# Kernel optimization log

Hardware: AMD Instinct MI355X
Metric: run time of the kernel (lower is better)

## Reference

```python
import jax, jax.numpy as jnp
import numpy as np

N_NODES = 50000
N_EDGES = 625000
D = 128          # hidden_dim
H = 8            # num_heads
DH = D // H      # head_dim
L = 4            # num_layers
F_IN = 64        # in_channels
G = 64           # num graphs
BETA = 1.0
EPS = 1e-5       # layernorm eps


def _seg_softmax(s, idx, n):
    # softmax of s over segments defined by idx (segments present in idx are never empty)
    m = jax.ops.segment_max(s, idx, num_segments=n)
    e = jnp.exp(s - m[idx])
    d = jax.ops.segment_sum(e, idx, num_segments=n)
    return e / d[idx]


def _ln(x, s, b):
    mu = jnp.mean(x, axis=-1, keepdims=True)
    var = jnp.var(x, axis=-1, keepdims=True)
    return (x - mu) / jnp.sqrt(var + EPS) * s + b


def _forward(x, edge_index, batch, node_W, node_b, cW1, cb1, cW2, cb2,
             qW, qb, kW, kb, vW, vb, oW, ob, bW, bb,
             f1W, f1b, f2W, f2b, n1s, n1b, n2s, n2b,
             outW1, outb1, outW2, outb2):
    N = x.shape[0]
    src, tgt = edge_index[0], edge_index[1]
    h = x @ node_W + node_b                              # [N, D]
    for l in range(L):
        # ---- dynamic curvature (attention-approximated Wasserstein) ----
        h_src, h_tgt = h[src], h[tgt]                    # [E, D]
        sim = jnp.sum(h_src * h_tgt, axis=-1) * BETA     # [E]
        alpha = _seg_softmax(sim, tgt, N)                # segment softmax over tgt
        dist = jnp.linalg.norm(h_src - h_tgt, axis=-1)   # [E]
        agg = jax.ops.segment_sum(alpha * dist, tgt, num_segments=N)
        curv = 1.0 - agg[tgt] / jnp.maximum(dist, 1e-6)  # [E]
        ce = jax.nn.relu(curv[:, None] @ cW1 + cb1) @ cW2 + cb2  # [E, D]
        # ---- CurvphormerLayer ----
        xn = _ln(h, n1s[l], n1b[l])
        q = (xn @ qW[l] + qb[l]).reshape(N, H, DH)
        k = (xn @ kW[l] + kb[l]).reshape(N, H, DH)
        v = (xn @ vW[l] + vb[l]).reshape(N, H, DH)
        scores = jnp.sum(q[src] * k[tgt], axis=-1) / (DH ** 0.5)  # [E, H]
        scores = scores + ce @ bW[l] + bb[l]                       # curvature bias
        probs = _seg_softmax(scores, tgt, N)                       # [E, H]
        msgs = (probs[..., None] * v[tgt]).reshape(-1, D)          # [E, D]
        aggm = jax.ops.segment_sum(msgs, src, num_segments=N)     # scatter to src
        h = h + (aggm @ oW[l] + ob[l])
        xn2 = _ln(h, n2s[l], n2b[l])
        h = h + (jax.nn.relu(xn2 @ f1W[l] + f1b[l]) @ f2W[l] + f2b[l])
    # ---- mean pool per graph ----
    counts = jnp.maximum(jax.ops.segment_sum(jnp.ones((N,), h.dtype), batch, num_segments=G), 1.0)
    g = jax.ops.segment_sum(h, batch, num_segments=G) / counts[:, None]
    return jax.nn.relu(g @ outW1 + outb1) @ outW2 + outb2


def setup_inputs() -> dict:
    keys = iter(jax.random.split(jax.random.key(0), 32))
    p = lambda shape, s=0.02: jax.random.normal(next(keys), shape, jnp.float32) * s
    x = jax.random.normal(next(keys), (N_NODES, F_IN), jnp.float32)
    edge_index = jax.random.randint(next(keys), (2, N_EDGES), 0, N_NODES)
    batch = jnp.sort(jax.random.randint(next(keys), (N_NODES,), 0, G))
    inp = {
        "x": x, "edge_index": edge_index, "batch": batch,
        "node_W": p((F_IN, D)), "node_b": p((D,)),
        "cW1": p((1, D)), "cb1": p((D,)), "cW2": p((D, D)), "cb2": p((D,)),
        "qW": p((L, D, D)), "qb": p((L, D)),
        "kW": p((L, D, D)), "kb": p((L, D)),
        "vW": p((L, D, D)), "vb": p((L, D)),
        "oW": p((L, D, D)), "ob": p((L, D)),
        "bW": p((L, D, H)), "bb": p((L, H)),
        "f1W": p((L, D, 4 * D)), "f1b": p((L, 4 * D)),
        "f2W": p((L, 4 * D, D)), "f2b": p((L, D)),
        "n1s": jnp.ones((L, D), jnp.float32), "n1b": jnp.zeros((L, D), jnp.float32),
        "n2s": jnp.ones((L, D), jnp.float32), "n2b": jnp.zeros((L, D), jnp.float32),
        "outW1": p((D, D // 2)), "outb1": p((D // 2,)),
        "outW2": p((D // 2, 1)), "outb2": p((1,)),
    }
    return inp


def reference(x, edge_index, batch, node_W, node_b, cW1, cb1, cW2, cb2,
              qW, qb, kW, kb, vW, vb, oW, ob, bW, bb,
              f1W, f1b, f2W, f2b, n1s, n1b, n2s, n2b,
              outW1, outb1, outW2, outb2):
    return _forward(x, edge_index, batch, node_W, node_b, cW1, cb1, cW2, cb2,
                    qW, qb, kW, kb, vW, vb, oW, ob, bW, bb,
                    f1W, f1b, f2W, f2b, n1s, n1b, n2s, n2b,
                    outW1, outb1, outW2, outb2)
```

## Files before the change

kernel.cpp:

```cpp
#include <hip/hip_runtime.h>

#define NN 50000
#define NE 625000
#define DD 128
#define HH 8
#define DHH 16
#define NL 4
#define FIN 64
#define NG 64
#define LN_EPS 1e-5f
#define NSEG 129
#define NT32 1563
#define NT64 782
#define NT4 12500
#define NBS 196
#define HLP 132

typedef __bf16 bf16x8_t __attribute__((ext_vector_type(8)));
typedef unsigned short ushort8_t __attribute__((ext_vector_type(8)));
typedef float f32x4_t __attribute__((ext_vector_type(4)));
union BF8 { ushort8_t u; bf16x8_t b; };

__device__ __forceinline__ void fma4(float4& a, float s, float4 w) {
  a.x = fmaf(s, w.x, a.x); a.y = fmaf(s, w.y, a.y);
  a.z = fmaf(s, w.z, a.z); a.w = fmaf(s, w.w, a.w);
}
__device__ __forceinline__ unsigned short f2bf(float f) {
  unsigned u = __float_as_uint(f);
  unsigned r = ((u >> 16) & 1u) + 0x7FFFu;
  return (unsigned short)((u + r) >> 16);
}
__device__ __forceinline__ float bf2f(unsigned short u) {
  return __uint_as_float((unsigned)u << 16);
}

__device__ __forceinline__ void ln_tile_bf32(const float* __restrict__ h, int nb,
                                             const float* __restrict__ sc,
                                             const float* __restrict__ bi,
                                             ushort* xbf) {
  int tid = threadIdx.x;
  int r = tid >> 4, l16 = tid & 15;
  int nr = nb + r; if (nr >= NN) nr = NN - 1;
  const float* hp = h + (size_t)nr * DD + l16 * 8;
  float4 a0 = *(const float4*)hp;
  float4 a1 = *(const float4*)(hp + 4);
  float sum = a0.x + a0.y + a0.z + a0.w + a1.x + a1.y + a1.z + a1.w;
  float sq  = a0.x*a0.x + a0.y*a0.y + a0.z*a0.z + a0.w*a0.w
            + a1.x*a1.x + a1.y*a1.y + a1.z*a1.z + a1.w*a1.w;
#pragma unroll
  for (int off = 8; off >= 1; off >>= 1) {
    sum += __shfl_xor(sum, off, 64);
    sq  += __shfl_xor(sq,  off, 64);
  }
  float mu   = sum * (1.0f / DD);
  float var  = sq * (1.0f / DD) - mu * mu;
  float rstd = rsqrtf(var + LN_EPS);
  int d0 = l16 * 8;
  float4 s0 = *(const float4*)(sc + d0), s1 = *(const float4*)(sc + d0 + 4);
  float4 b0 = *(const float4*)(bi + d0), b1 = *(const float4*)(bi + d0 + 4);
  ushort8_t u;
  u[0] = f2bf((a0.x - mu) * rstd * s0.x + b0.x);
  u[1] = f2bf((a0.y - mu) * rstd * s0.y + b0.y);
  u[2] = f2bf((a0.z - mu) * rstd * s0.z + b0.z);
  u[3] = f2bf((a0.w - mu) * rstd * s0.w + b0.w);
  u[4] = f2bf((a1.x - mu) * rstd * s1.x + b1.x);
  u[5] = f2bf((a1.y - mu) * rstd * s1.y + b1.y);
  u[6] = f2bf((a1.z - mu) * rstd * s1.z + b1.z);
  u[7] = f2bf((a1.w - mu) * rstd * s1.w + b1.w);
  int off = (r * 256 + l16 * 16) ^ ((r & 7) << 4);
  *(ushort8_t*)((char*)xbf + off) = u;
}

__global__ __launch_bounds__(256) void k_node_proj(const float* __restrict__ x,
                                                   const float* __restrict__ W,
                                                   const float* __restrict__ b,
                                                   float* __restrict__ h) {
  __shared__ float Wl[FIN * DD];
  __shared__ float xt[32][FIN];
  int tid = threadIdx.x;
  int nb = blockIdx.x * 32;
  for (int i = tid * 4; i < FIN * DD; i += 1024)
    *(float4*)&Wl[i] = *(const float4*)(W + i);
  for (int i = tid * 4; i < 32 * FIN; i += 1024) {
    int row = i >> 6, cc = i & 63;
    int node = nb + row; if (node >= NN) node = NN - 1;
    *(float4*)&xt[row][cc] = *(const float4*)(x + (size_t)node * FIN + cc);
  }
  __syncthreads();
  int c4 = (tid & 31) * 4;
  int r0 = (tid >> 5) * 4;
  float4 bv = *(const float4*)(b + c4);
  float4 a0 = bv, a1 = bv, a2 = bv, a3 = bv;
  for (int k = 0; k < FIN; k++) {
    float4 wv = *(const float4*)&Wl[k * DD + c4];
    fma4(a0, xt[r0][k], wv);
    fma4(a1, xt[r0 + 1][k], wv);
    fma4(a2, xt[r0 + 2][k], wv);
    fma4(a3, xt[r0 + 3][k], wv);
  }
  int n0 = nb + r0;
  if (n0 < NN)     *(float4*)(h + (size_t)n0 * DD + c4) = a0;
  if (n0 + 1 < NN) *(float4*)(h + (size_t)(n0 + 1) * DD + c4) = a1;
  if (n0 + 2 < NN) *(float4*)(h + (size_t)(n0 + 2) * DD + c4) = a2;
  if (n0 + 3 < NN) *(float4*)(h + (size_t)(n0 + 3) * DD + c4) = a3;
}

__global__ __launch_bounds__(256) void k_edge1(const int* __restrict__ src_s, const int* __restrict__ tgt_s,
                                               const float* __restrict__ h, float* __restrict__ sim,
                                               float* __restrict__ dist) {
  int gid = blockIdx.x * 256 + threadIdx.x;
  int e = gid >> 4;
  if (e >= NE) return;
  int j = gid & 15;
  int s = src_s[e], t = tgt_s[e];
  const float4* ap = (const float4*)(h + (size_t)s * DD + j * 8);
  const float4* bp = (const float4*)(h + (size_t)t * DD + j * 8);
  float4 a0 = ap[0], a1 = ap[1];
  float4 b0 = bp[0], b1 = bp[1];
  float dot = 0.f, sq = 0.f;
  dot = fmaf(a0.x, b0.x, dot); dot = fmaf(a0.y, b0.y, dot);
  dot = fmaf(a0.z, b0.z, dot); dot = fmaf(a0.w, b0.w, dot);
  dot = fmaf(a1.x, b1.x, dot); dot = fmaf(a1.y, b1.y, dot);
  dot = fmaf(a1.z, b1.z, dot); dot = fmaf(a1.w, b1.w, dot);
  float d0 = a0.x - b0.x, d1 = a0.y - b0.y, d2 = a0.z - b0.z, d3 = a0.w - b0.w;
  float d4 = a1.x - b1.x, d5 = a1.y - b1.y, d6 = a1.z - b1.z, d7 = a1.w - b1.w;
  sq = fmaf(d0, d0, sq); sq = fmaf(d1, d1, sq); sq = fmaf(d2, d2, sq); sq = fmaf(d3, d3, sq);
  sq = fmaf(d4, d4, sq); sq = fmaf(d5, d5, sq); sq = fmaf(d6, d6, sq); sq = fmaf(d7, d7, sq);
#pragma unroll
  for (int off = 8; off >= 1; off >>= 1) {
    dot += __shfl_xor(dot, off, 64);
    sq  += __shfl_xor(sq,  off, 64);
  }
  if (j == 0) {
    sim[e]  = dot;
    dist[e] = sqrtf(sq);
  }
}

__global__ __launch_bounds__(256) void k_curva(const int* __restrict__ rowstart_t,
    const int* __restrict__ eid_t, const float* __restrict__ sim,
    const float* __restrict__ dist, float* __restrict__ aggv) {
  int node = blockIdx.x * 32 + (threadIdx.x >> 3);
  if (node >= NN) return;
  int j = threadIdx.x & 7;
  int rs = rowstart_t[node], re = rowstart_t[node + 1];
  float m = -3.4e38f;
  for (int i = rs + j; i < re; i += 8) m = fmaxf(m, sim[eid_t[i]]);
#pragma unroll
  for (int off = 1; off <= 4; off <<= 1) m = fmaxf(m, __shfl_xor(m, off, 64));
  float den = 0.f, nd = 0.f;
  for (int i = rs + j; i < re; i += 8) {
    int e = eid_t[i];
    float ev = expf(sim[e] - m);
    den += ev;
    nd = fmaf(ev, dist[e], nd);
  }
#pragma unroll
  for (int off = 1; off <= 4; off <<= 1) {
    den += __shfl_xor(den, off, 64);
    nd  += __shfl_xor(nd,  off, 64);
  }
  if (j == 0) aggv[node] = den > 0.f ? nd / den : 0.f;
}

__global__ __launch_bounds__(512) void k_ln_qkv(const float* __restrict__ h,
    const float* __restrict__ n1s_l, const float* __restrict__ n1b_l,
    const ushort* __restrict__ qkvT_l,
    const float* __restrict__ qb_l, const float* __restrict__ kb_l, const float* __restrict__ vb_l,
    ushort* __restrict__ q, ushort* __restrict__ kk, ushort* __restrict__ v) {
  __shared__ __align__(16) ushort xbf[32 * DD];
  int nb = blockIdx.x * 32;
  ln_tile_bf32(h, nb, n1s_l, n1b_l, xbf);
  __syncthreads();
  int lane = threadIdx.x & 63;
  int w = threadIdx.x >> 6;
  int g = lane >> 4, c = lane & 15;
  int xr = (c & 7) << 4;
  char* xb = (char*)xbf;
  BF8 a[2][4];
#pragma unroll
  for (int nt = 0; nt < 2; nt++)
#pragma unroll
    for (int kt = 0; kt < 4; kt++)
      a[nt][kt].u = *(ushort8_t*)(xb + (((nt * 16 + c) * 256 + kt * 64 + g * 16) ^ xr));
#pragma unroll
  for (int ti = 0; ti < 3; ti++) {
    int t = w * 3 + ti;
    int m = t >> 3;
    int colb = (t & 7) * 16;
    const float* bias = (m == 0 ? qb_l : (m == 1 ? kb_l : vb_l));
    float4 bv = *(const float4*)(bias + colb + g * 4);
    f32x4_t acc0 = {bv.x, bv.y, bv.z, bv.w};
    f32x4_t acc1 = acc0;
    const ushort* wp = qkvT_l + (size_t)(m * DD + colb + c) * DD + g * 8;
#pragma unroll
    for (int kt = 0; kt < 4; kt++) {
      BF8 b; b.u = *(const ushort8_t*)(wp + kt * 32);
      acc0 = __builtin_amdgcn_mfma_f32_16x16x32_bf16(b.b, a[0][kt].b, acc0, 0, 0, 0);
      acc1 = __builtin_amdgcn_mfma_f32_16x16x32_bf16(b.b, a[1][kt].b, acc1, 0, 0, 0);
    }
    ushort* out = (m == 0 ? q : (m == 1 ? kk : v));
    int n0 = nb + c;
    if (n0 < NN) {
      ushort4 o; o.x = f2bf(acc0[0]); o.y = f2bf(acc0[1]); o.z = f2bf(acc0[2]); o.w = f2bf(acc0[3]);
      *(ushort4*)(out + (size_t)n0 * DD + colb + g * 4) = o;
    }
    int n1 = nb + 16 + c;
    if (n1 < NN) {
      ushort4 o; o.x = f2bf(acc1[0]); o.y = f2bf(acc1[1]); o.z = f2bf(acc1[2]); o.w = f2bf(acc1[3]);
      *(ushort4*)(out + (size_t)n1 * DD + colb + g * 4) = o;
    }
  }
}

__global__ __launch_bounds__(256) void k_scores_sm(const int* __restrict__ src_s,
    const int* __restrict__ rowstart_t, const int* __restrict__ eid_t,
    const ushort* __restrict__ q, const ushort* __restrict__ k,
    const float* __restrict__ dist, const float* __restrict__ aggv,
    const float* __restrict__ bp_g,
    const float* __restrict__ slope_l, const float* __restrict__ inter_l,
    float* __restrict__ escore, float2* __restrict__ msd) {
  __shared__ float lsl[NSEG * HH], lin[NSEG * HH], bp[DD];
  int tid = threadIdx.x;
  for (int idx = tid; idx < NSEG * HH; idx += 256) { lsl[idx] = slope_l[idx]; lin[idx] = inter_l[idx]; }
  if (tid < DD) bp[tid] = bp_g[tid];
  __syncthreads();
  int node = blockIdx.x * 4 + (tid >> 6);
  if (node >= NN) return;
  int lane = tid & 63;
  int hh = lane & 7;
  int eidx = lane >> 3;
  int rs = rowstart_t[node], re = rowstart_t[node + 1];
  float av = aggv[node];
  const ushort8_t* kp = (const ushort8_t*)(k + (size_t)node * DD + hh * DHH);
  ushort8_t k0 = kp[0], k1 = kp[1];
  float m = -3.4e38f, ssum = 0.f;
  for (int i = rs + eidx; i < re; i += 8) {
    int e = eid_t[i];
    int s = src_s[e];
    float dd = dist[e];
    const ushort8_t* qp = (const ushort8_t*)(q + (size_t)s * DD + hh * DHH);
    ushort8_t q0 = qp[0], q1 = qp[1];
    float curv = 1.0f - av / fmaxf(dd, 1e-6f);
    int lo = 0, hi = DD;
    while (lo < hi) { int mid = (lo + hi) >> 1; if (bp[mid] < curv) lo = mid + 1; else hi = mid; }
    float bias = fmaf(lsl[lo * HH + hh], curv, lin[lo * HH + hh]);
    float dot = 0.f;
#pragma unroll
    for (int jj = 0; jj < 8; jj++) dot = fmaf(bf2f(q0[jj]), bf2f(k0[jj]), dot);
#pragma unroll
    for (int jj = 0; jj < 8; jj++) dot = fmaf(bf2f(q1[jj]), bf2f(k1[jj]), dot);
    float sc = dot * 0.25f + bias;
    escore[e * HH + hh] = sc;
    float mn = fmaxf(m, sc);
    ssum = ssum * expf(m - mn) + expf(sc - mn);
    m = mn;
  }
#pragma unroll
  for (int off = 8; off <= 32; off <<= 1) {
    float m2 = __shfl_xor(m, off, 64);
    float s2 = __shfl_xor(ssum, off, 64);
    float M = fmaxf(m, m2);
    ssum = ssum * expf(m - M) + s2 * expf(m2 - M);
    m = M;
  }
  if (eidx == 0) {
    float2 o; o.x = m; o.y = ssum > 0.f ? 1.0f / ssum : 0.f;
    msd[(size_t)node * HH + hh] = o;
  }
}

__global__ __launch_bounds__(256) void k_agg(const int* __restrict__ tgt_s,
    const int* __restrict__ rowstart,
    const float* __restrict__ escore, const float2* __restrict__ msd,
    const ushort* __restrict__ v, ushort* __restrict__ aggmb) {
  int wave = (blockIdx.x * 256 + threadIdx.x) >> 6;
  int lane = threadIdx.x & 63;
  int rs = rowstart[wave], re = rowstart[wave + 1];
  int hh = lane >> 3;
  int d = lane * 2;
  float a0 = 0.f, a1 = 0.f;
  int i = rs;
  for (; i + 4 <= re; i += 4) {
    int t0 = tgt_s[i], t1 = tgt_s[i + 1], t2 = tgt_s[i + 2], t3 = tgt_s[i + 3];
    float e0 = escore[(i    ) * HH + hh];
    float e1 = escore[(i + 1) * HH + hh];
    float e2 = escore[(i + 2) * HH + hh];
    float e3 = escore[(i + 3) * HH + hh];
    float2 m0 = msd[(size_t)t0 * HH + hh], m1 = msd[(size_t)t1 * HH + hh];
    float2 m2 = msd[(size_t)t2 * HH + hh], m3 = msd[(size_t)t3 * HH + hh];
    ushort2 v0 = *(const ushort2*)(v + (size_t)t0 * DD + d);
    ushort2 v1 = *(const ushort2*)(v + (size_t)t1 * DD + d);
    ushort2 v2 = *(const ushort2*)(v + (size_t)t2 * DD + d);
    ushort2 v3 = *(const ushort2*)(v + (size_t)t3 * DD + d);
    float p0 = expf(e0 - m0.x) * m0.y;
    float p1 = expf(e1 - m1.x) * m1.y;
    float p2 = expf(e2 - m2.x) * m2.y;
    float p3 = expf(e3 - m3.x) * m3.y;
    a0 = fmaf(p0, bf2f(v0.x), a0); a1 = fmaf(p0, bf2f(v0.y), a1);
    a0 = fmaf(p1, bf2f(v1.x), a0); a1 = fmaf(p1, bf2f(v1.y), a1);
    a0 = fmaf(p2, bf2f(v2.x), a0); a1 = fmaf(p2, bf2f(v2.y), a1);
    a0 = fmaf(p3, bf2f(v3.x), a0); a1 = fmaf(p3, bf2f(v3.y), a1);
  }
  for (; i < re; i++) {
    int t = tgt_s[i];
    float2 md = msd[(size_t)t * HH + hh];
    float prob = expf(escore[i * HH + hh] - md.x) * md.y;
    ushort2 vv = *(const ushort2*)(v + (size_t)t * DD + d);
    a0 = fmaf(prob, bf2f(vv.x), a0);
    a1 = fmaf(prob, bf2f(vv.y), a1);
  }
  ushort2 o; o.x = f2bf(a0); o.y = f2bf(a1);
  *(ushort2*)(aggmb + (size_t)wave * DD + d) = o;
}

__global__ __launch_bounds__(512) void k_attn_ffn(const ushort* __restrict__ aggmb,
    const ushort* __restrict__ oT_l, const float* __restrict__ ob_l,
    const float* __restrict__ n2s_l, const float* __restrict__ n2b_l,
    const ushort* __restrict__ f1T_l, const float* __restrict__ f1b_l,
    const ushort* __restrict__ f2T_l, const float* __restrict__ f2b_l,
    float* __restrict__ h) {
  __shared__ float hL[64 * HLP];
  __shared__ __align__(16) char ubuf[64 * 128 * 2];
  char* xb = ubuf;
  char* tb = ubuf;
  int nb = blockIdx.x * 64;
  int tid = threadIdx.x;
  int lane = tid & 63, w = tid >> 6;
  int g = lane >> 4, c = lane & 15;
  int colb = w * 16;
  int xr = (c & 7) << 4;
  {
    float4 obv = *(const float4*)(ob_l + colb + g * 4);
    const ushort* wp = oT_l + (size_t)(colb + c) * DD + g * 8;
    BF8 b0, b1, b2, b3;
    b0.u = *(const ushort8_t*)(wp);
    b1.u = *(const ushort8_t*)(wp + 32);
    b2.u = *(const ushort8_t*)(wp + 64);
    b3.u = *(const ushort8_t*)(wp + 96);
#pragma unroll
    for (int nt = 0; nt < 4; nt++) {
      int node = nb + nt * 16 + c;
      int na = node < NN ? node : NN - 1;
      const ushort* ap = aggmb + (size_t)na * DD + g * 8;
      BF8 a0, a1, a2, a3;
      a0.u = *(const ushort8_t*)(ap);
      a1.u = *(const ushort8_t*)(ap + 32);
      a2.u = *(const ushort8_t*)(ap + 64);
      a3.u = *(const ushort8_t*)(ap + 96);
      f32x4_t acc = {obv.x, obv.y, obv.z, obv.w};
      acc = __builtin_amdgcn_mfma_f32_16x16x32_bf16(b0.b, a0.b, acc, 0, 0, 0);
      acc = __builtin_amdgcn_mfma_f32_16x16x32_bf16(b1.b, a1.b, acc, 0, 0, 0);
      acc = __builtin_amdgcn_mfma_f32_16x16x32_bf16(b2.b, a2.b, acc, 0, 0, 0);
      acc = __builtin_amdgcn_mfma_f32_16x16x32_bf16(b3.b, a3.b, acc, 0, 0, 0);
      float4 hv = *(const float4*)(h + (size_t)na * DD + colb + g * 4);
      hv.x += acc[0]; hv.y += acc[1]; hv.z += acc[2]; hv.w += acc[3];
      *(float4*)&hL[(nt * 16 + c) * HLP + colb + g * 4] = hv;
    }
  }
  __syncthreads();
  {
    int l16 = tid & 15;
    int d0 = l16 * 8;
    float4 s0 = *(const float4*)(n2s_l + d0), s1 = *(const float4*)(n2s_l + d0 + 4);
    float4 bb0 = *(const float4*)(n2b_l + d0), bb1 = *(const float4*)(n2b_l + d0 + 4);
#pragma unroll
    for (int p = 0; p < 2; p++) {
      int r = p * 32 + (tid >> 4);
      const float* hp = &hL[r * HLP + d0];
      float4 a0 = *(const float4*)hp;
      float4 a1 = *(const float4*)(hp + 4);
      float sum = a0.x + a0.y + a0.z + a0.w + a1.x + a1.y + a1.z + a1.w;
      float sq  = a0.x*a0.x + a0.y*a0.y + a0.z*a0.z + a0.w*a0.w
                + a1.x*a1.x + a1.y*a1.y + a1.z*a1.z + a1.w*a1.w;
#pragma unroll
      for (int off = 8; off >= 1; off >>= 1) {
        sum += __shfl_xor(sum, off, 64);
        sq  += __shfl_xor(sq,  off, 64);
      }
      float mu   = sum * (1.0f / DD);
      float var  = sq * (1.0f / DD) - mu * mu;
      float rstd = rsqrtf(var + LN_EPS);
      ushort8_t u;
      u[0] = f2bf((a0.x - mu) * rstd * s0.x + bb0.x);
      u[1] = f2bf((a0.y - mu) * rstd * s0.y + bb0.y);
      u[2] = f2bf((a0.z - mu) * rstd * s0.z + bb0.z);
      u[3] = f2bf((a0.w - mu) * rstd * s0.w + bb0.w);
      u[4] = f2bf((a1.x - mu) * rstd * s1.x + bb1.x);
      u[5] = f2bf((a1.y - mu) * rstd * s1.y + bb1.y);
      u[6] = f2bf((a1.z - mu) * rstd * s1.z + bb1.z);
      u[7] = f2bf((a1.w - mu) * rstd * s1.w + bb1.w);
      int off = (r * 256 + l16 * 16) ^ ((r & 7) << 4);
      *(ushort8_t*)(xb + off) = u;
    }
  }
  __syncthreads();
  BF8 a[4][4];
#pragma unroll
  for (int nt = 0; nt < 4; nt++)
#pragma unroll
    for (int kt = 0; kt < 4; kt++)
      a[nt][kt].u = *(ushort8_t*)(xb + (((nt * 16 + c) * 256 + kt * 64 + g * 16) ^ xr));
  __syncthreads();
  float4 bv2 = *(const float4*)(f2b_l + colb + g * 4);
  f32x4_t o0 = {bv2.x, bv2.y, bv2.z, bv2.w};
  f32x4_t o1 = o0, o2 = o0, o3 = o0;
#pragma unroll
  for (int ch = 0; ch < 4; ch++) {
    if (ch) __syncthreads();
    {
      int col = ch * 128 + w * 16;
      float4 bv = *(const float4*)(f1b_l + col + g * 4);
      f32x4_t ac0 = {bv.x, bv.y, bv.z, bv.w};
      f32x4_t ac1 = ac0, ac2 = ac0, ac3 = ac0;
      const ushort* wp = f1T_l + (size_t)(col + c) * DD + g * 8;
#pragma unroll
      for (int kt = 0; kt < 4; kt++) {
        BF8 b; b.u = *(const ushort8_t*)(wp + kt * 32);
        ac0 = __builtin_amdgcn_mfma_f32_16x16x32_bf16(b.b, a[0][kt].b, ac0, 0, 0, 0);
        ac1 = __builtin_amdgcn_mfma_f32_16x16x32_bf16(b.b, a[1][kt].b, ac1, 0, 0, 0);
        ac2 = __builtin_amdgcn_mfma_f32_16x16x32_bf16(b.b, a[2][kt].b, ac2, 0, 0, 0);
        ac3 = __builtin_amdgcn_mfma_f32_16x16x32_bf16(b.b, a[3][kt].b, ac3, 0, 0, 0);
      }
      int colL = (w * 16 + g * 4) * 2;
      {
        int row = c;
        ushort4 o4; o4.x = f2bf(fmaxf(ac0[0], 0.f)); o4.y = f2bf(fmaxf(ac0[1], 0.f));
        o4.z = f2bf(fmaxf(ac0[2], 0.f)); o4.w = f2bf(fmaxf(ac0[3], 0.f));
        *(ushort4*)(tb + ((row * 256 + colL) ^ ((row & 7) << 4))) = o4;
      }
      {
        int row = 16 + c;
        ushort4 o4; o4.x = f2bf(fmaxf(ac1[0], 0.f)); o4.y = f2bf(fmaxf(ac1[1], 0.f));
        o4.z = f2bf(fmaxf(ac1[2], 0.f)); o4.w = f2bf(fmaxf(ac1[3], 0.f));
        *(ushort4*)(tb + ((row * 256 + colL) ^ ((row & 7) << 4))) = o4;
      }
      {
        int row = 32 + c;
        ushort4 o4; o4.x = f2bf(fmaxf(ac2[0], 0.f)); o4.y = f2bf(fmaxf(ac2[1], 0.f));
        o4.z = f2bf(fmaxf(ac2[2], 0.f)); o4.w = f2bf(fmaxf(ac2[3], 0.f));
        *(ushort4*)(tb + ((row * 256 + colL) ^ ((row & 7) << 4))) = o4;
      }
      {
        int row = 48 + c;
        ushort4 o4; o4.x = f2bf(fmaxf(ac3[0], 0.f)); o4.y = f2bf(fmaxf(ac3[1], 0.f));
        o4.z = f2bf(fmaxf(ac3[2], 0.f)); o4.w = f2bf(fmaxf(ac3[3], 0.f));
        *(ushort4*)(tb + ((row * 256 + colL) ^ ((row & 7) << 4))) = o4;
      }
    }
    __syncthreads();
    const ushort* wp2 = f2T_l + (size_t)(colb + c) * 512 + ch * 128 + g * 8;
#pragma unroll
    for (int kt = 0; kt < 4; kt++) {
      BF8 b; b.u = *(const ushort8_t*)(wp2 + kt * 32);
      BF8 t0; t0.u = *(ushort8_t*)(tb + (((c) * 256 + kt * 64 + g * 16) ^ xr));
      BF8 t1; t1.u = *(ushort8_t*)(tb + (((16 + c) * 256 + kt * 64 + g * 16) ^ xr));
      BF8 t2; t2.u = *(ushort8_t*)(tb + (((32 + c) * 256 + kt * 64 + g * 16) ^ xr));
      BF8 t3; t3.u = *(ushort8_t*)(tb + (((48 + c) * 256 + kt * 64 + g * 16) ^ xr));
      o0 = __builtin_amdgcn_mfma_f32_16x16x32_bf16(b.b, t0.b, o0, 0, 0, 0);
      o1 = __builtin_amdgcn_mfma_f32_16x16x32_bf16(b.b, t1.b, o1, 0, 0, 0);
      o2 = __builtin_amdgcn_mfma_f32_16x16x32_bf16(b.b, t2.b, o2, 0, 0, 0);
      o3 = __builtin_amdgcn_mfma_f32_16x16x32_bf16(b.b, t3.b, o3, 0, 0, 0);
    }
  }
  {
    int node = nb + c;
    if (node < NN) {
      const float* lp = &hL[c * HLP + colb + g * 4];
      float4 hv = *(const float4*)lp;
      hv.x += o0[0]; hv.y += o0[1]; hv.z += o0[2]; hv.w += o0[3];
      *(float4*)(h + (size_t)node * DD + colb + g * 4) = hv;
    }
  }
  {
    int node = nb + 16 + c;
    if (node < NN) {
      const float* lp = &hL[(16 + c) * HLP + colb + g * 4];
      float4 hv = *(const float4*)lp;
      hv.x += o1[0]; hv.y += o1[1]; hv.z += o1[2]; hv.w += o1[3];
      *(float4*)(h + (size_t)node * DD + colb + g * 4) = hv;
    }
  }
  {
    int node = nb + 32 + c;
    if (node < NN) {
      const float* lp = &hL[(32 + c) * HLP + colb + g * 4];
      float4 hv = *(const float4*)lp;
      hv.x += o2[0]; hv.y += o2[1]; hv.z += o2[2]; hv.w += o2[3];
      *(float4*)(h + (size_t)node * DD + colb + g * 4) = hv;
    }
  }
  {
    int node = nb + 48 + c;
    if (node < NN) {
      const float* lp = &hL[(48 + c) * HLP + colb + g * 4];
      float4 hv = *(const float4*)lp;
      hv.x += o3[0]; hv.y += o3[1]; hv.z += o3[2]; hv.w += o3[3];
      *(float4*)(h + (size_t)node * DD + colb + g * 4) = hv;
    }
  }
}

template <int K, int C>
__global__ void k_wt(const float* __restrict__ W, ushort* __restrict__ WT, int nm, int dstride) {
  int idx = blockIdx.x * 256 + threadIdx.x;
  if (idx >= K * C * nm) return;
  int mi = idx / (K * C), rem = idx - mi * (K * C);
  int cc = rem / K, kk2 = rem - cc * K;
  WT[(size_t)mi * dstride + cc * K + kk2] = f2bf(W[(size_t)mi * K * C + (size_t)kk2 * C + cc]);
}

__global__ void k_hist(const int* __restrict__ idxs, int* __restrict__ cnt) {
  int e = blockIdx.x * 256 + threadIdx.x;
  if (e < NE) atomicAdd(cnt + idxs[e], 1);
}

__global__ __launch_bounds__(256) void k_scan_blk(const int* __restrict__ cnt, int* __restrict__ bsum) {
  __shared__ int red[256];
  int tid = threadIdx.x;
  int idx = blockIdx.x * 256 + tid;
  red[tid] = (idx < NN) ? cnt[idx] : 0;
  __syncthreads();
  for (int off = 128; off >= 1; off >>= 1) {
    if (tid < off) red[tid] += red[tid + off];
    __syncthreads();
  }
  if (tid == 0) bsum[blockIdx.x] = red[0];
}

__global__ __launch_bounds__(256) void k_scan_top(const int* __restrict__ bsum,
                                                  int* __restrict__ boff, int* __restrict__ rowstart) {
  __shared__ int ps[256];
  int t = threadIdx.x;
  int v = (t < NBS) ? bsum[t] : 0;
  ps[t] = v;
  __syncthreads();
  for (int off = 1; off < 256; off <<= 1) {
    int x = (t >= off) ? ps[t - off] : 0;
    __syncthreads();
    ps[t] += x;
    __syncthreads();
  }
  boff[t] = ps[t] - v;
  if (t == 255) rowstart[NN] = ps[255];
}

__global__ __launch_bounds__(256) void k_scan_fin(const int* __restrict__ cnt,
                                                  const int* __restrict__ boff, int* __restrict__ rowstart) {
  __shared__ int ps[256];
  int t = threadIdx.x;
  int idx = blockIdx.x * 256 + t;
  int v = (idx < NN) ? cnt[idx] : 0;
  ps[t] = v;
  __syncthreads();
  for (int off = 1; off < 256; off <<= 1) {
    int x = (t >= off) ? ps[t - off] : 0;
    __syncthreads();
    ps[t] += x;
    __syncthreads();
  }
  if (idx < NN) rowstart[idx] = boff[blockIdx.x] + ps[t] - v;
}

__global__ void k_fill(const int* __restrict__ src, const int* __restrict__ tgt,
                       const int* __restrict__ rowstart,
                       int* __restrict__ cur, int* __restrict__ src_s, int* __restrict__ tgt_s) {
  int e = blockIdx.x * 256 + threadIdx.x;
  if (e >= NE) return;
  int s = src[e];
  int p = atomicAdd(cur + s, 1);
  int pos = rowstart[s] + p;
  src_s[pos] = s;
  tgt_s[pos] = tgt[e];
}

__global__ void k_fill_t(const int* __restrict__ tgt_s, const int* __restrict__ rowstart_t,
                         int* __restrict__ cur_t, int* __restrict__ eid_t) {
  int i = blockIdx.x * 256 + threadIdx.x;
  if (i >= NE) return;
  int t = tgt_s[i];
  int p = atomicAdd(cur_t + t, 1);
  eid_t[rowstart_t[t] + p] = i;
}

__global__ __launch_bounds__(64) void k_mbias_par(const float* __restrict__ cW2, const float* __restrict__ cb2,
                                                  const float* __restrict__ bW, const float* __restrict__ bb,
                                                  float* __restrict__ M, float* __restrict__ base) {
  int bid = blockIdx.x;
  int l = bid >> 7, d = bid & 127;
  int lane = threadIdx.x;
  int hh = lane >> 3, j0 = lane & 7;
  const float* bWl = bW + (size_t)l * DD * HH;
  float acc = 0.f;
#pragma unroll
  for (int t = 0; t < 16; t++) {
    int k = j0 + t * 8;
    acc = fmaf(cW2[d * DD + k], bWl[k * HH + hh], acc);
  }
#pragma unroll
  for (int off = 1; off <= 4; off <<= 1) acc += __shfl_xor(acc, off, 64);
  if (j0 == 0) M[(size_t)l * DD * HH + d * HH + hh] = acc;
  if (d == 0) {
    float bacc = 0.f;
#pragma unroll
    for (int t = 0; t < 16; t++) {
      int k = j0 + t * 8;
      bacc = fmaf(cb2[k], bWl[k * HH + hh], bacc);
    }
#pragma unroll
    for (int off = 1; off <= 4; off <<= 1) bacc += __shfl_xor(bacc, off, 64);
    if (j0 == 0) base[l * HH + hh] = bacc + bb[l * HH + hh];
  }
}

__global__ __launch_bounds__(128) void k_bp(const float* __restrict__ cW1, const float* __restrict__ cb1,
                                            float* __restrict__ bpg, int* __restrict__ posg) {
  __shared__ float x[DD], bp[DD];
  int tid = threadIdx.x;
  float c1v = cW1[tid], cbv = cb1[tid];
  x[tid] = (c1v == 0.f) ? __builtin_inff() : (-cbv / c1v);
  __syncthreads();
  float xv = x[tid]; int p = 0;
  for (int j = 0; j < DD; j++) {
    float xj = x[j];
    if (xj < xv || (xj == xv && j < tid)) p++;
  }
  bp[p] = xv;
  posg[tid] = p;
  __syncthreads();
  bpg[tid] = bp[tid];
}

__global__ __launch_bounds__(64) void k_pwl_tab(const float* __restrict__ cW1, const float* __restrict__ cb1,
    const int* __restrict__ posg, const float* __restrict__ Mb, const float* __restrict__ basel,
    float* __restrict__ slopeg, float* __restrict__ interg) {
  int bid = blockIdx.x;
  int l = bid / NSEG, s = bid - l * NSEG;
  int lane = threadIdx.x;
  int hh = lane >> 3, j0 = lane & 7;
  const float* M = Mb + (size_t)l * DD * HH;
  float sl = 0.f, in = 0.f;
#pragma unroll
  for (int t = 0; t < 16; t++) {
    int d = j0 + t * 8;
    float cv = cW1[d], cbv = cb1[d];
    int p = posg[d];
    bool act = (cv == 0.f) ? (cbv > 0.f) : ((cv > 0.f) ? (p < s) : (p >= s));
    float m = act ? M[d * HH + hh] : 0.f;
    sl = fmaf(cv, m, sl);
    in = fmaf(cbv, m, in);
  }
#pragma unroll
  for (int off = 1; off <= 4; off <<= 1) {
    sl += __shfl_xor(sl, off, 64);
    in += __shfl_xor(in, off, 64);
  }
  if (j0 == 0) {
    size_t o = (size_t)l * NSEG * HH + s * HH + hh;
    slopeg[o] = sl;
    interg[o] = in + basel[l * HH + hh];
  }
}

__global__ void k_bounds(const int* __restrict__ batch, int* __restrict__ gstart, int* __restrict__ gend) {
  int n = blockIdx.x * 256 + threadIdx.x;
  if (n >= NN) return;
  int b = batch[n];
  if (n == 0 || batch[n - 1] != b) gstart[b] = n;
  if (n == NN - 1 || batch[n + 1] != b) gend[b] = n + 1;
}

__global__ __launch_bounds__(256) void k_pool_part(const float* __restrict__ h,
    const int* __restrict__ batch, float* __restrict__ gpool) {
  int tid = threadIdx.x;
  int d = tid & 127, sub = tid >> 7;
  int n0 = blockIdx.x * 256;
  int nend = n0 + 256; if (nend > NN) nend = NN;
  float run = 0.f; int gcur = -1;
  for (int n = n0 + sub; n < nend; n += 2) {
    int g = batch[n];
    if (g != gcur) {
      if (gcur >= 0) atomicAdd(gpool + (size_t)gcur * DD + d, run);
      run = 0.f; gcur = g;
    }
    run += h[(size_t)n * DD + d];
  }
  if (gcur >= 0) atomicAdd(gpool + (size_t)gcur * DD + d, run);
}

__global__ __launch_bounds__(256) void k_head(const float* __restrict__ gpool,
    const int* __restrict__ gstart, const int* __restrict__ gend,
    const float* __restrict__ W1, const float* __restrict__ b1,
    const float* __restrict__ W2, const float* __restrict__ b2, float* __restrict__ out) {
  __shared__ float mid[NG * 64];
  int tid = threadIdx.x;
  for (int idx = tid; idx < NG * 64; idx += 256) {
    int g = idx >> 6, j = idx & 63;
    int cnt = gend[g] - gstart[g]; if (cnt < 1) cnt = 1;
    float rc = 1.0f / (float)cnt;
    float acc = 0.f;
    for (int d = 0; d < DD; d++) acc = fmaf(gpool[g * DD + d], W1[d * 64 + j], acc);
    mid[idx] = fmaxf(fmaf(acc, rc, b1[j]), 0.f);
  }
  __syncthreads();
  if (tid < NG) {
    float acc = b2[0];
    for (int j = 0; j < 64; j++) acc = fmaf(mid[tid * 64 + j], W2[j], acc);
    out[tid] = acc;
  }
}

extern "C" void kernel_launch(void* const* d_in, const int* in_sizes, int n_in,
                              void* d_out, int out_size, void* d_ws, size_t ws_size,
                              hipStream_t stream) {
  const float* x      = (const float*)d_in[0];
  const int*   ei     = (const int*)d_in[1];
  const int*   batch  = (const int*)d_in[2];
  const float* node_W = (const float*)d_in[3];
  const float* node_b = (const float*)d_in[4];
  const float* cW1    = (const float*)d_in[5];
  const float* cb1    = (const float*)d_in[6];
  const float* cW2    = (const float*)d_in[7];
  const float* cb2    = (const float*)d_in[8];
  const float* qW     = (const float*)d_in[9];
  const float* qb     = (const float*)d_in[10];
  const float* kW     = (const float*)d_in[11];
  const float* kb     = (const float*)d_in[12];
  const float* vW     = (const float*)d_in[13];
  const float* vb     = (const float*)d_in[14];
  const float* oW     = (const float*)d_in[15];
  const float* ob     = (const float*)d_in[16];
  const float* bW     = (const float*)d_in[17];
  const float* bb     = (const float*)d_in[18];
  const float* f1W    = (const float*)d_in[19];
  const float* f1b    = (const float*)d_in[20];
  const float* f2W    = (const float*)d_in[21];
  const float* f2b    = (const float*)d_in[22];
  const float* n1s    = (const float*)d_in[23];
  const float* n1b    = (const float*)d_in[24];
  const float* n2s    = (const float*)d_in[25];
  const float* n2b    = (const float*)d_in[26];
  const float* outW1  = (const float*)d_in[27];
  const float* outb1  = (const float*)d_in[28];
  const float* outW2  = (const float*)d_in[29];
  const float* outb2  = (const float*)d_in[30];

  const int* src = ei;
  const int* tgt = ei + NE;

  char* wp = (char*)d_ws;
  auto alloc = [&](size_t bytes) { void* p = (void*)wp; wp += (bytes + 255) & ~(size_t)255; return p; };
  float*    h       = (float*)alloc((size_t)NN * DD * 4);
  ushort*   q       = (ushort*)alloc((size_t)NN * DD * 2);
  ushort*   kk      = (ushort*)alloc((size_t)NN * DD * 2);
  ushort*   v       = (ushort*)alloc((size_t)NN * DD * 2);
  ushort*   aggmb   = (ushort*)alloc((size_t)NN * DD * 2);
  float*    sim     = (float*)alloc((size_t)NE * 4);
  float*    dist    = (float*)alloc((size_t)NE * 4);
  float*    escore  = (float*)alloc((size_t)NE * HH * 4);
  float2*   msd     = (float2*)alloc((size_t)NN * HH * 8);
  float*    aggv    = (float*)alloc((size_t)NN * 4);
  float*    Mb      = (float*)alloc((size_t)NL * DD * HH * 4);
  float*    basel   = (float*)alloc((size_t)NL * HH * 4);
  float*    bpg     = (float*)alloc((size_t)DD * 4);
  int*      posg    = (int*)alloc((size_t)DD * 4);
  float*    slopeg  = (float*)alloc((size_t)NL * NSEG * HH * 4);
  float*    interg  = (float*)alloc((size_t)NL * NSEG * HH * 4);
  int*      rowstart= (int*)alloc((size_t)(NN + 1) * 4);
  int*      rowstart_t = (int*)alloc((size_t)(NN + 1) * 4);
  int*      eid_t   = (int*)alloc((size_t)NE * 4);
  int*      src_s   = (int*)alloc((size_t)NE * 4);
  int*      tgt_s   = (int*)alloc((size_t)NE * 4);
  int*      cnt     = (int*)alloc((size_t)NN * 4);
  int*      cur     = (int*)alloc((size_t)NN * 4);
  int*      cnt_t   = (int*)alloc((size_t)NN * 4);
  int*      cur_t   = (int*)alloc((size_t)NN * 4);
  int*      bsum    = (int*)alloc((size_t)NBS * 4);
  int*      boff    = (int*)alloc((size_t)256 * 4);
  int*      gstart  = (int*)alloc((size_t)NG * 4);
  int*      gend    = (int*)alloc((size_t)NG * 4);
  float*    gpool   = (float*)alloc((size_t)NG * DD * 4);
  ushort*   qkvT    = (ushort*)alloc((size_t)NL * 3 * DD * DD * 2);
  ushort*   oT      = (ushort*)alloc((size_t)NL * DD * DD * 2);
  ushort*   f1T     = (ushort*)alloc((size_t)NL * DD * 512 * 2);
  ushort*   f2T     = (ushort*)alloc((size_t)NL * 512 * DD * 2);
  (void)in_sizes; (void)n_in; (void)out_size; (void)ws_size;

  hipMemsetAsync(cnt, 0, NN * 4, stream);
  hipMemsetAsync(cur, 0, NN * 4, stream);
  hipMemsetAsync(cnt_t, 0, NN * 4, stream);
  hipMemsetAsync(cur_t, 0, NN * 4, stream);
  hipMemsetAsync(gstart, 0, NG * 4, stream);
  hipMemsetAsync(gend, 0, NG * 4, stream);
  hipMemsetAsync(gpool, 0, NG * DD * 4, stream);
  k_hist<<<(NE + 255) / 256, 256, 0, stream>>>(src, cnt);
  k_scan_blk<<<NBS, 256, 0, stream>>>(cnt, bsum);
  k_scan_top<<<1, 256, 0, stream>>>(bsum, boff, rowstart);
  k_scan_fin<<<NBS, 256, 0, stream>>>(cnt, boff, rowstart);
  k_fill<<<(NE + 255) / 256, 256, 0, stream>>>(src, tgt, rowstart, cur, src_s, tgt_s);
  k_hist<<<(NE + 255) / 256, 256, 0, stream>>>(tgt, cnt_t);
  k_scan_blk<<<NBS, 256, 0, stream>>>(cnt_t, bsum);
  k_scan_top<<<1, 256, 0, stream>>>(bsum, boff, rowstart_t);
  k_scan_fin<<<NBS, 256, 0, stream>>>(cnt_t, boff, rowstart_t);
  k_fill_t<<<(NE + 255) / 256, 256, 0, stream>>>(tgt_s, rowstart_t, cur_t, eid_t);
  k_mbias_par<<<NL * DD, 64, 0, stream>>>(cW2, cb2, bW, bb, Mb, basel);
  k_bp<<<1, 128, 0, stream>>>(cW1, cb1, bpg, posg);
  k_pwl_tab<<<NL * NSEG, 64, 0, stream>>>(cW1, cb1, posg, Mb, basel, slopeg, interg);
  k_bounds<<<(NN + 255) / 256, 256, 0, stream>>>(batch, gstart, gend);
  k_wt<DD, DD><<<(NL * DD * DD + 255) / 256, 256, 0, stream>>>(qW, qkvT,               NL, 3 * DD * DD);
  k_wt<DD, DD><<<(NL * DD * DD + 255) / 256, 256, 0, stream>>>(kW, qkvT + DD * DD,     NL, 3 * DD * DD);
  k_wt<DD, DD><<<(NL * DD * DD + 255) / 256, 256, 0, stream>>>(vW, qkvT + 2 * DD * DD, NL, 3 * DD * DD);
  k_wt<DD, DD><<<(NL * DD * DD + 255) / 256, 256, 0, stream>>>(oW, oT, NL, DD * DD);
  k_wt<DD, 512><<<(NL * DD * 512 + 255) / 256, 256, 0, stream>>>(f1W, f1T, NL, DD * 512);
  k_wt<512, DD><<<(NL * DD * 512 + 255) / 256, 256, 0, stream>>>(f2W, f2T, NL, DD * 512);
  k_node_proj<<<NT32, 256, 0, stream>>>(x, node_W, node_b, h);

  for (int l = 0; l < NL; l++) {
    k_edge1<<<(NE * 16 + 255) / 256, 256, 0, stream>>>(src_s, tgt_s, h, sim, dist);
    k_curva<<<NT32, 256, 0, stream>>>(rowstart_t, eid_t, sim, dist, aggv);
    k_ln_qkv<<<NT32, 512, 0, stream>>>(h, n1s + l * DD, n1b + l * DD,
        qkvT + (size_t)l * 3 * DD * DD,
        qb + l * DD, kb + l * DD, vb + l * DD, q, kk, v);
    k_scores_sm<<<NT4, 256, 0, stream>>>(src_s, rowstart_t, eid_t, q, kk,
        dist, aggv, bpg,
        slopeg + (size_t)l * NSEG * HH, interg + (size_t)l * NSEG * HH,
        escore, msd);
    k_agg<<<NN / 4, 256, 0, stream>>>(tgt_s, rowstart, escore, msd, v, aggmb);
    k_attn_ffn<<<NT64, 512, 0, stream>>>(aggmb, oT + (size_t)l * DD * DD, ob + l * DD,
        n2s + l * DD, n2b + l * DD,
        f1T + (size_t)l * DD * 512, f1b + (size_t)l * 4 * DD,
        f2T + (size_t)l * 512 * DD, f2b + l * DD, h);
  }
  k_pool_part<<<(NN + 255) / 256, 256, 0, stream>>>(h, batch, gpool);
  k_head<<<1, 256, 0, stream>>>(gpool, gstart, gend, outW1, outb1, outW2, outb2, (float*)d_out);
}
```

Before: 1.321 ms.

## Fuse next layer's LayerNorm and QKV projection into attention-FFN epilogue

```diff
diff --git a/kernel.cpp b/kernel.cpp
--- a/kernel.cpp
+++ b/kernel.cpp
@@ -319,7 +319,12 @@
     const float* __restrict__ n2s_l, const float* __restrict__ n2b_l,
     const ushort* __restrict__ f1T_l, const float* __restrict__ f1b_l,
     const ushort* __restrict__ f2T_l, const float* __restrict__ f2b_l,
-    float* __restrict__ h) {
+    float* __restrict__ h,
+    int do_qkv,
+    const float* __restrict__ n1s_n, const float* __restrict__ n1b_n,
+    const ushort* __restrict__ qkvT_n,
+    const float* __restrict__ qb_n, const float* __restrict__ kb_n, const float* __restrict__ vb_n,
+    ushort* __restrict__ q, ushort* __restrict__ kk, ushort* __restrict__ v) {
   __shared__ float hL[64 * HLP];
   __shared__ __align__(16) char ubuf[64 * 128 * 2];
   char* xb = ubuf;
@@ -464,39 +469,127 @@
     }
   }
   {
+    float* lp = &hL[c * HLP + colb + g * 4];
+    float4 hv = *(const float4*)lp;
+    hv.x += o0[0]; hv.y += o0[1]; hv.z += o0[2]; hv.w += o0[3];
+    *(float4*)lp = hv;
     int node = nb + c;
-    if (node < NN) {
-      const float* lp = &hL[c * HLP + colb + g * 4];
-      float4 hv = *(const float4*)lp;
-      hv.x += o0[0]; hv.y += o0[1]; hv.z += o0[2]; hv.w += o0[3];
-      *(float4*)(h + (size_t)node * DD + colb + g * 4) = hv;
-    }
+    if (node < NN) *(float4*)(h + (size_t)node * DD + colb + g * 4) = hv;
   }
   {
+    float* lp = &hL[(16 + c) * HLP + colb + g * 4];
+    float4 hv = *(const float4*)lp;
+    hv.x += o1[0]; hv.y += o1[1]; hv.z += o1[2]; hv.w += o1[3];
+    *(float4*)lp = hv;
     int node = nb + 16 + c;
-    if (node < NN) {
-      const float* lp = &hL[(16 + c) * HLP + colb + g * 4];
-      float4 hv = *(const float4*)lp;
-      hv.x += o1[0]; hv.y += o1[1]; hv.z += o1[2]; hv.w += o1[3];
-      *(float4*)(h + (size_t)node * DD + colb + g * 4) = hv;
-    }
+    if (node < NN) *(float4*)(h + (size_t)node * DD + colb + g * 4) = hv;
   }
   {
+    float* lp = &hL[(32 + c) * HLP + colb + g * 4];
+    float4 hv = *(const float4*)lp;
+    hv.x += o2[0]; hv.y += o2[1]; hv.z += o2[2]; hv.w += o2[3];
+    *(float4*)lp = hv;
     int node = nb + 32 + c;
-    if (node < NN) {
-      const float* lp = &hL[(32 + c) * HLP + colb + g * 4];
-      float4 hv = *(const float4*)lp;
-      hv.x += o2[0]; hv.y += o2[1]; hv.z += o2[2]; hv.w += o2[3];
-      *(float4*)(h + (size_t)node * DD + colb + g * 4) = hv;
-    }
+    if (node < NN) *(float4*)(h + (size_t)node * DD + colb + g * 4) = hv;
   }
   {
+    float* lp = &hL[(48 + c) * HLP + colb + g * 4];
+    float4 hv = *(const float4*)lp;
+    hv.x += o3[0]; hv.y += o3[1]; hv.z += o3[2]; hv.w += o3[3];
+    *(float4*)lp = hv;
     int node = nb + 48 + c;
-    if (node < NN) {
-      const float* lp = &hL[(48 + c) * HLP + colb + g * 4];
-      float4 hv = *(const float4*)lp;
-      hv.x += o3[0]; hv.y += o3[1]; hv.z += o3[2]; hv.w += o3[3];
-      *(float4*)(h + (size_t)node * DD + colb + g * 4) = hv;
+    if (node < NN) *(float4*)(h + (size_t)node * DD + colb + g * 4) = hv;
+  }
+  if (!do_qkv) return;
+  __syncthreads();
+  {
+    int l16 = tid & 15;
+    int d0 = l16 * 8;
+    float4 s0 = *(const float4*)(n1s_n + d0), s1 = *(const float4*)(n1s_n + d0 + 4);
+    float4 bb0 = *(const float4*)(n1b_n + d0), bb1 = *(const float4*)(n1b_n + d0 + 4);
+#pragma unroll
+    for (int p = 0; p < 2; p++) {
+      int r = p * 32 + (tid >> 4);
+      const float* hp = &hL[r * HLP + d0];
+      float4 a0 = *(const float4*)hp;
+      float4 a1 = *(const float4*)(hp + 4);
+      float sum = a0.x + a0.y + a0.z + a0.w + a1.x + a1.y + a1.z + a1.w;
+      float sq  = a0.x*a0.x + a0.y*a0.y + a0.z*a0.z + a0.w*a0.w
+                + a1.x*a1.x + a1.y*a1.y + a1.z*a1.z + a1.w*a1.w;
+#pragma unroll
+      for (int off = 8; off >= 1; off >>= 1) {
+        sum += __shfl_xor(sum, off, 64);
+        sq  += __shfl_xor(sq,  off, 64);
+      }
+      float mu   = sum * (1.0f / DD);
+      float var  = sq * (1.0f / DD) - mu * mu;
+      float rstd = rsqrtf(var + LN_EPS);
+      ushort8_t u;
+      u[0] = f2bf((a0.x - mu) * rstd * s0.x + bb0.x);
+      u[1] = f2bf((a0.y - mu) * rstd * s0.y + bb0.y);
+      u[2] = f2bf((a0.z - mu) * rstd * s0.z + bb0.z);
+      u[3] = f2bf((a0.w - mu) * rstd * s0.w + bb0.w);
+      u[4] = f2bf((a1.x - mu) * rstd * s1.x + bb1.x);
+      u[5] = f2bf((a1.y - mu) * rstd * s1.y + bb1.y);
+      u[6] = f2bf((a1.z - mu) * rstd * s1.z + bb1.z);
+      u[7] = f2bf((a1.w - mu) * rstd * s1.w + bb1.w);
+      int off = (r * 256 + l16 * 16) ^ ((r & 7) << 4);
+      *(ushort8_t*)(xb + off) = u;
+    }
+  }
+  __syncthreads();
+  BF8 aq[4][4];
+#pragma unroll
+  for (int nt = 0; nt < 4; nt++)
+#pragma unroll
+    for (int kt = 0; kt < 4; kt++)
+      aq[nt][kt].u = *(ushort8_t*)(xb + (((nt * 16 + c) * 256 + kt * 64 + g * 16) ^ xr));
+#pragma unroll
+  for (int ti = 0; ti < 3; ti++) {
+    int t = w * 3 + ti;
+    int m = t >> 3;
+    int colq = (t & 7) * 16;
+    const float* bias = (m == 0 ? qb_n : (m == 1 ? kb_n : vb_n));
+    float4 bv = *(const float4*)(bias + colq + g * 4);
+    f32x4_t ac0 = {bv.x, bv.y, bv.z, bv.w};
+    f32x4_t ac1 = ac0, ac2 = ac0, ac3 = ac0;
+    const ushort* wp = qkvT_n + (size_t)(m * DD + colq + c) * DD + g * 8;
+#pragma unroll
+    for (int kt = 0; kt < 4; kt++) {
+      BF8 b; b.u = *(const ushort8_t*)(wp + kt * 32);
+      ac0 = __builtin_amdgcn_mfma_f32_16x16x32_bf16(b.b, aq[0][kt].b, ac0, 0, 0, 0);
+      ac1 = __builtin_amdgcn_mfma_f32_16x16x32_bf16(b.b, aq[1][kt].b, ac1, 0, 0, 0);
+      ac2 = __builtin_amdgcn_mfma_f32_16x16x32_bf16(b.b, aq[2][kt].b, ac2, 0, 0, 0);
+      ac3 = __builtin_amdgcn_mfma_f32_16x16x32_bf16(b.b, aq[3][kt].b, ac3, 0, 0, 0);
+    }
+    ushort* out = (m == 0 ? q : (m == 1 ? kk : v));
+    {
+      int node = nb + c;
+      if (node < NN) {
+        ushort4 o; o.x = f2bf(ac0[0]); o.y = f2bf(ac0[1]); o.z = f2bf(ac0[2]); o.w = f2bf(ac0[3]);
+        *(ushort4*)(out + (size_t)node * DD + colq + g * 4) = o;
+      }
+    }
+    {
+      int node = nb + 16 + c;
+      if (node < NN) {
+        ushort4 o; o.x = f2bf(ac1[0]); o.y = f2bf(ac1[1]); o.z = f2bf(ac1[2]); o.w = f2bf(ac1[3]);
+        *(ushort4*)(out + (size_t)node * DD + colq + g * 4) = o;
+      }
+    }
+    {
+      int node = nb + 32 + c;
+      if (node < NN) {
+        ushort4 o; o.x = f2bf(ac2[0]); o.y = f2bf(ac2[1]); o.z = f2bf(ac2[2]); o.w = f2bf(ac2[3]);
+        *(ushort4*)(out + (size_t)node * DD + colq + g * 4) = o;
+      }
+    }
+    {
+      int node = nb + 48 + c;
+      if (node < NN) {
+        ushort4 o; o.x = f2bf(ac3[0]); o.y = f2bf(ac3[1]); o.z = f2bf(ac3[2]); o.w = f2bf(ac3[3]);
+        *(ushort4*)(out + (size_t)node * DD + colq + g * 4) = o;
+      }
     }
   }
 }
@@ -814,22 +907,26 @@
   k_wt<DD, 512><<<(NL * DD * 512 + 255) / 256, 256, 0, stream>>>(f1W, f1T, NL, DD * 512);
   k_wt<512, DD><<<(NL * DD * 512 + 255) / 256, 256, 0, stream>>>(f2W, f2T, NL, DD * 512);
   k_node_proj<<<NT32, 256, 0, stream>>>(x, node_W, node_b, h);
+  k_ln_qkv<<<NT32, 512, 0, stream>>>(h, n1s, n1b, qkvT, qb, kb, vb, q, kk, v);
 
   for (int l = 0; l < NL; l++) {
     k_edge1<<<(NE * 16 + 255) / 256, 256, 0, stream>>>(src_s, tgt_s, h, sim, dist);
     k_curva<<<NT32, 256, 0, stream>>>(rowstart_t, eid_t, sim, dist, aggv);
-    k_ln_qkv<<<NT32, 512, 0, stream>>>(h, n1s + l * DD, n1b + l * DD,
-        qkvT + (size_t)l * 3 * DD * DD,
-        qb + l * DD, kb + l * DD, vb + l * DD, q, kk, v);
     k_scores_sm<<<NT4, 256, 0, stream>>>(src_s, rowstart_t, eid_t, q, kk,
         dist, aggv, bpg,
         slopeg + (size_t)l * NSEG * HH, interg + (size_t)l * NSEG * HH,
         escore, msd);
     k_agg<<<NN / 4, 256, 0, stream>>>(tgt_s, rowstart, escore, msd, v, aggmb);
+    int ln = l < NL - 1 ? l + 1 : l;
     k_attn_ffn<<<NT64, 512, 0, stream>>>(aggmb, oT + (size_t)l * DD * DD, ob + l * DD,
         n2s + l * DD, n2b + l * DD,
         f1T + (size_t)l * DD * 512, f1b + (size_t)l * 4 * DD,
-        f2T + (size_t)l * 512 * DD, f2b + l * DD, h);
+        f2T + (size_t)l * 512 * DD, f2b + l * DD, h,
+        (l < NL - 1) ? 1 : 0,
+        n1s + ln * DD, n1b + ln * DD,
+        qkvT + (size_t)ln * 3 * DD * DD,
+        qb + ln * DD, kb + ln * DD, vb + ln * DD,
+        q, kk, v);
   }
   k_pool_part<<<(NN + 255) / 256, 256, 0, stream>>>(h, batch, gpool);
   k_head<<<1, 256, 0, stream>>>(gpool, gstart, gend, outW1, outb1, outW2, outb2, (float*)d_out);
```

Measured after the change: 1.322 ms. About the same (+0.1%).
